# Kernel optimization log

Measured on AMD Instinct MI355X. Metric: run time of the kernel, lower is better.

Reference implementation:

```python
import jax, jax.numpy as jnp
import numpy as np


def _erode3d(v):
    # torch: -F.max_pool3d(-v, 3, stride=1, padding=1)  == 3x3x3 min-pool, SAME padding
    return -jax.lax.reduce_window(-v, -jnp.inf, jax.lax.max,
                                  (1, 1, 3, 3, 3), (1, 1, 1, 1, 1), 'SAME')


def _chamfer(pred, gt):
    # pred [B,N,3], gt [B,M,3]; squared-euclidean pairwise via |p|^2 + |g|^2 - 2 p.g
    p2 = jnp.sum(pred * pred, axis=-1)            # [B,N]
    g2 = jnp.sum(gt * gt, axis=-1)                # [B,M]
    cross = jnp.einsum('bnd,bmd->bnm', pred, gt)  # [B,N,M]
    d = p2[:, :, None] + g2[:, None, :] - 2.0 * cross
    return jnp.mean(jnp.min(d, axis=2)) + jnp.mean(jnp.min(d, axis=1))


def _cldice(pred_volume, gt_volume, smooth=1e-5):
    pred_skel = _erode3d(jax.nn.sigmoid(pred_volume))
    gt_skel = _erode3d(gt_volume)
    inter = jnp.sum(pred_skel * gt_skel, axis=(2, 3, 4))
    psum = jnp.sum(pred_skel, axis=(2, 3, 4))
    gsum = jnp.sum(gt_skel, axis=(2, 3, 4))
    dice = (2.0 * inter + smooth) / (psum + gsum + smooth)
    return 1.0 - jnp.mean(dice)


def _depth_loss(pred, gt, mask, alpha=0.1, beta=10.0):
    B = pred.shape[0]
    # SILog
    g = (jnp.log(pred + alpha) - jnp.log(gt + alpha)).reshape(B, -1)
    g_mean = jnp.mean(g, axis=1)
    g_var = jnp.mean(g * g, axis=1) - g_mean * g_mean  # biased var
    silog = 10.0 * jnp.mean(g_var) + beta * jnp.mean(g_mean ** 2)
    # gradient L1
    pgx = jnp.abs(pred[:, :-1, :] - pred[:, 1:, :])
    pgy = jnp.abs(pred[:, :, :-1] - pred[:, :, 1:])
    ggx = jnp.abs(gt[:, :-1, :] - gt[:, 1:, :])
    ggy = jnp.abs(gt[:, :, :-1] - gt[:, :, 1:])
    grad_l1 = jnp.mean(jnp.abs(pgx - ggx)) + jnp.mean(jnp.abs(pgy - ggy))
    # masked L1
    mask_l1 = jnp.sum(jnp.abs(pred - gt) * mask) / (jnp.sum(mask) + 1e-8)
    return silog + grad_l1 + mask_l1


def setup_inputs() -> dict:
    key = jax.random.key(0)
    ks = jax.random.split(key, 6)
    B, N, M = 2, 8192, 8192
    D, H, W = 64, 128, 128
    DH, DW = 512, 512
    return {
        'pred_centers': jax.random.normal(ks[0], (B, N, 3), jnp.float32),
        'pred_volume': jax.random.normal(ks[1], (B, 1, D, H, W), jnp.float32),
        'pred_depth': jax.random.uniform(ks[2], (B, DH, DW), jnp.float32),
        'gt_points': jax.random.normal(ks[3], (B, M, 3), jnp.float32),
        'gt_volume': jax.random.uniform(ks[4], (B, 1, D, H, W), jnp.float32),
        'gt_depth': jax.random.uniform(ks[5], (B, DH, DW), jnp.float32),
        'depth_mask': jnp.ones((B, DH, DW), jnp.float32),
        'iteration': 10000,
    }


def reference(pred_centers, pred_volume, pred_depth, gt_points, gt_volume,
              gt_depth, depth_mask, iteration):
    gamma1_base, gamma2, gamma3 = 2.0, 0.5, 0.01
    gamma1 = gamma1_base * np.log(max(int(iteration), 1) / 20000.0)
    chamfer = _chamfer(pred_centers, gt_points)
    cldice = _cldice(pred_volume, gt_volume)
    dloss = _depth_loss(pred_depth, gt_depth, depth_mask)
    total = gamma1 * chamfer + gamma2 * cldice + gamma3 * dloss
    return total
```

## Files before the change

kernel.cpp:

```cpp
#include <hip/hip_runtime.h>
#include <math.h>

#define B 2
#define N 8192
#define M 8192
#define NPTS (B*N)
#define VD 64
#define VH 128
#define VW 128
#define VVOX (VD*VH*VW)
#define DHH 512
#define DWW 512
#define DPIX (DHH*DWW)

#define OFF_PACK_P 0
#define OFF_PACK_G 65536
#define OFF_WH_P   131072
#define OFF_WH_G   2228224
#define OFF_CHPART 4325376
#define OFF_PCL    5373952
#define OFF_PDE    5375488
#define OFF_PCH    5377024

__device__ __forceinline__ float blockSum(float v, volatile float* sm) {
    #pragma unroll
    for (int o = 32; o > 0; o >>= 1) v += __shfl_down(v, o, 64);
    int lane = threadIdx.x & 63, wid = threadIdx.x >> 6;
    __syncthreads();
    if (lane == 0) sm[wid] = v;
    __syncthreads();
    return sm[0] + sm[1] + sm[2] + sm[3];
}

__device__ __forceinline__ float min3f(float a, float b, float c) {
    return fminf(a, fminf(b, c));
}

__global__ __launch_bounds__(256) void k_pack(const float* __restrict__ pc,
                                              const float* __restrict__ gp,
                                              float* ws) {
    int i = blockIdx.x * 256 + threadIdx.x;
    if (i >= NPTS) return;
    float x = pc[3*i], y = pc[3*i+1], z = pc[3*i+2];
    ((float4*)(ws + OFF_PACK_P))[i] = make_float4(x, y, z, x*x + y*y + z*z);
    x = gp[3*i]; y = gp[3*i+1]; z = gp[3*i+2];
    ((float4*)(ws + OFF_PACK_G))[i] = make_float4(x, y, z, x*x + y*y + z*z);
}

#define QT 8
#define SEGS 32
#define TSEG (M/SEGS)
__global__ __launch_bounds__(256) void k_chamfer(float* ws) {
    __shared__ float4 tt[TSEG];
    const float4* packP = (const float4*)(ws + OFF_PACK_P);
    const float4* packG = (const float4*)(ws + OFF_PACK_G);
    unsigned int bid = blockIdx.x;
    int dir  = bid >> 8;
    int rem  = bid & 255;
    int seg  = rem >> 3;
    int qblk = rem & 7;
    const float4* Q = dir ? packG : packP;
    const float4* T = dir ? packP : packG;

    int qbase = qblk * (256*QT);
    int b = qbase >> 13;

    tt[threadIdx.x] = T[b*M + seg*TSEG + threadIdx.x];

    float nx[QT], ny[QT], nz[QT], q2[QT], dmin[QT];
    #pragma unroll
    for (int k = 0; k < QT; ++k) {
        float4 qv = Q[qbase + k*256 + threadIdx.x];
        nx[k] = -2.f*qv.x; ny[k] = -2.f*qv.y; nz[k] = -2.f*qv.z;
        q2[k] = qv.w; dmin[k] = INFINITY;
    }
    __syncthreads();

    #pragma unroll 4
    for (int j = 0; j < TSEG; ++j) {
        float4 tv = tt[j];
        #pragma unroll
        for (int k = 0; k < QT; ++k) {
            float d = fmaf(tv.x, nx[k], fmaf(tv.y, ny[k], fmaf(tv.z, nz[k], tv.w)));
            dmin[k] = fminf(dmin[k], d);
        }
    }
    float* part = ws + OFF_CHPART + dir*(SEGS*NPTS) + seg*NPTS + qbase;
    #pragma unroll
    for (int k = 0; k < QT; ++k)
        part[k*256 + threadIdx.x] = dmin[k] + q2[k];
}

__global__ __launch_bounds__(256) void k_redmin(float* ws) {
    __shared__ float sm[4];
    int r   = blockIdx.x;
    int dir = r >> 5;
    int blk = r & 31;
    const float* base = ws + OFF_CHPART + dir*(SEGS*NPTS) + blk*512;
    float s = 0.f;
    #pragma unroll
    for (int u = 0; u < 2; ++u) {
        int t = u*256 + threadIdx.x;
        float m = INFINITY;
        #pragma unroll
        for (int sg = 0; sg < SEGS; ++sg) m = fminf(m, base[sg*NPTS + t]);
        s += m;
    }
    float a = blockSum(s, sm);
    if (threadIdx.x == 0) ws[OFF_PCH + r] = a;
}

__global__ __launch_bounds__(256) void k_erodeA(const float* __restrict__ pv,
                                                const float* __restrict__ gv,
                                                float* ws) {
    int r0 = blockIdx.x * 8 + (threadIdx.x >> 5);
    int q  = threadIdx.x & 31;
    int w  = q * 4;
    int b  = r0 >> 13;
    int rb = r0 & 8191;
    int d  = rb >> 7;
    int h  = rb & 127;
    int rowOff = b*VVOX + d*(VH*VW) + h*VW;
    int up = (h > 0)   ? -VW : 0;
    int dn = (h < 127) ?  VW : 0;

    float4 om[2];
    const float* vols[2] = {pv, gv};
    #pragma unroll
    for (int a = 0; a < 2; ++a) {
        const float* row = vols[a] + rowOff;
        float4 acc = make_float4(INFINITY, INFINITY, INFINITY, INFINITY);
        #pragma unroll
        for (int rr = 0; rr < 3; ++rr) {
            const float* rw = row + (rr == 0 ? up : (rr == 2 ? dn : 0));
            float4 c = *(const float4*)(rw + w);
            float l = (q > 0)  ? rw[w-1] : c.x;
            float r = (q < 31) ? rw[w+4] : c.w;
            acc.x = fminf(acc.x, min3f(l,   c.x, c.y));
            acc.y = fminf(acc.y, min3f(c.x, c.y, c.z));
            acc.z = fminf(acc.z, min3f(c.y, c.z, c.w));
            acc.w = fminf(acc.w, min3f(c.z, c.w, r));
        }
        om[a] = acc;
    }
    ((float4*)(ws + OFF_WH_P + rowOff))[q] = om[0];
    ((float4*)(ws + OFF_WH_G + rowOff))[q] = om[1];
}

__global__ __launch_bounds__(256) void k_erodeB(float* ws) {
    __shared__ float sm[4];
    const float4* whP = (const float4*)(ws + OFF_WH_P);
    const float4* whG = (const float4*)(ws + OFF_WH_G);
    int b   = blockIdx.x >> 8;
    int blk = blockIdx.x & 255;
    float li = 0.f, lp = 0.f, lg = 0.f;
    #pragma unroll
    for (int k = 0; k < 4; ++k) {
        int f4 = b*(VVOX/4) + (blk*4 + k)*256 + threadIdx.x;
        int d  = (f4 >> 12) & 63;
        int up = (d > 0)  ? -4096 : 0;
        int dn = (d < 63) ?  4096 : 0;
        float4 p0 = whP[f4+up], p1 = whP[f4], p2 = whP[f4+dn];
        float4 g0 = whG[f4+up], g1 = whG[f4], g2 = whG[f4+dn];
        float4 mp = make_float4(min3f(p0.x,p1.x,p2.x), min3f(p0.y,p1.y,p2.y),
                                min3f(p0.z,p1.z,p2.z), min3f(p0.w,p1.w,p2.w));
        float4 mg = make_float4(min3f(g0.x,g1.x,g2.x), min3f(g0.y,g1.y,g2.y),
                                min3f(g0.z,g1.z,g2.z), min3f(g0.w,g1.w,g2.w));
        float4 ps = make_float4(1.f/(1.f+__expf(-mp.x)), 1.f/(1.f+__expf(-mp.y)),
                                1.f/(1.f+__expf(-mp.z)), 1.f/(1.f+__expf(-mp.w)));
        li += ps.x*mg.x + ps.y*mg.y + ps.z*mg.z + ps.w*mg.w;
        lp += ps.x + ps.y + ps.z + ps.w;
        lg += mg.x + mg.y + mg.z + mg.w;
    }
    float a;
    float* part = ws + OFF_PCL;
    a = blockSum(li, sm); if (threadIdx.x == 0) part[          blockIdx.x] = a;
    a = blockSum(lp, sm); if (threadIdx.x == 0) part[512     + blockIdx.x] = a;
    a = blockSum(lg, sm); if (threadIdx.x == 0) part[1024    + blockIdx.x] = a;
}

__global__ __launch_bounds__(256) void k_depth(const float* __restrict__ pd,
                                               const float* __restrict__ gd,
                                               const float* __restrict__ mk,
                                               float* ws) {
    __shared__ float sm[4];
    int b   = blockIdx.x >> 7;
    int blk = blockIdx.x & 127;
    const float* pb = pd + b * DPIX;
    const float* gb = gd + b * DPIX;
    const float* mb = mk + b * DPIX;
    float sg = 0, sg2 = 0, gx = 0, gy = 0, num = 0, den = 0;
    #pragma unroll
    for (int k = 0; k < 8; ++k) {
        int idx = (blk*8 + k)*256 + threadIdx.x;
        int h = idx >> 9;
        int w = idx & 511;
        float p = pb[idx], g = gb[idx], m = mb[idx];
        float lgv = logf(p + 0.1f) - logf(g + 0.1f);
        sg += lgv; sg2 += lgv * lgv;
        if (h < DHH - 1) {
            float p2 = pb[idx + DWW], g2 = gb[idx + DWW];
            gx += fabsf(fabsf(p - p2) - fabsf(g - g2));
        }
        if (w < DWW - 1) {
            float p2 = pb[idx + 1], g2 = gb[idx + 1];
            gy += fabsf(fabsf(p - p2) - fabsf(g - g2));
        }
        num += fabsf(p - g) * m;
        den += m;
    }
    float a;
    float* part = ws + OFF_PDE;
    a = blockSum(sg,  sm); if (threadIdx.x == 0) part[       blockIdx.x] = a;
    a = blockSum(sg2, sm); if (threadIdx.x == 0) part[256  + blockIdx.x] = a;
    a = blockSum(gx,  sm); if (threadIdx.x == 0) part[512  + blockIdx.x] = a;
    a = blockSum(gy,  sm); if (threadIdx.x == 0) part[768  + blockIdx.x] = a;
    a = blockSum(num, sm); if (threadIdx.x == 0) part[1024 + blockIdx.x] = a;
    a = blockSum(den, sm); if (threadIdx.x == 0) part[1280 + blockIdx.x] = a;
}

__device__ __forceinline__ float sumRange(const float* p, int n, volatile float* sm) {
    float s = 0.f;
    for (int t = threadIdx.x; t < n; t += 256) s += p[t];
    return blockSum(s, sm);
}

__global__ __launch_bounds__(256) void k_final(const float* ws, const int* iter,
                                               float* out) {
    __shared__ float sm[4];
    float sch = sumRange(ws + OFF_PCH, 64, sm);
    float i0  = sumRange(ws + OFF_PCL,        256, sm);
    float i1  = sumRange(ws + OFF_PCL + 256,  256, sm);
    float p0  = sumRange(ws + OFF_PCL + 512,  256, sm);
    float p1  = sumRange(ws + OFF_PCL + 768,  256, sm);
    float g0  = sumRange(ws + OFF_PCL + 1024, 256, sm);
    float g1  = sumRange(ws + OFF_PCL + 1280, 256, sm);
    float sg0 = sumRange(ws + OFF_PDE,        128, sm);
    float sg1 = sumRange(ws + OFF_PDE + 128,  128, sm);
    float s20 = sumRange(ws + OFF_PDE + 256,  128, sm);
    float s21 = sumRange(ws + OFF_PDE + 384,  128, sm);
    float gx  = sumRange(ws + OFF_PDE + 512,  256, sm);
    float gy  = sumRange(ws + OFF_PDE + 768,  256, sm);
    float num = sumRange(ws + OFF_PDE + 1024, 256, sm);
    float den = sumRange(ws + OFF_PDE + 1280, 256, sm);
    if (threadIdx.x != 0) return;

    float chamfer = sch / (float)NPTS;
    float dsum = (2.f*i0 + 1e-5f) / (p0 + g0 + 1e-5f)
               + (2.f*i1 + 1e-5f) / (p1 + g1 + 1e-5f);
    float cldice = 1.f - 0.5f * dsum;
    float silog = 0.f;
    {
        float gm = sg0 / (float)DPIX;
        float gv = s20 / (float)DPIX - gm*gm;
        silog += 10.f*0.5f*gv + 10.f*0.5f*gm*gm;
        gm = sg1 / (float)DPIX;
        gv = s21 / (float)DPIX - gm*gm;
        silog += 10.f*0.5f*gv + 10.f*0.5f*gm*gm;
    }
    float grad_l1 = gx / (float)(B*(DHH-1)*DWW) + gy / (float)(B*DHH*(DWW-1));
    float mask_l1 = num / (den + 1e-8f);
    float dloss = silog + grad_l1 + mask_l1;
    int it = iter[0]; if (it < 1) it = 1;
    float gamma1 = 2.f * logf((float)it / 20000.f);
    out[0] = gamma1 * chamfer + 0.5f * cldice + 0.01f * dloss;
}

extern "C" void kernel_launch(void* const* d_in, const int* in_sizes, int n_in,
                              void* d_out, int out_size, void* d_ws, size_t ws_size,
                              hipStream_t stream) {
    const float* pc  = (const float*)d_in[0];
    const float* pv  = (const float*)d_in[1];
    const float* pd  = (const float*)d_in[2];
    const float* gp  = (const float*)d_in[3];
    const float* gvv = (const float*)d_in[4];
    const float* gd  = (const float*)d_in[5];
    const float* mk  = (const float*)d_in[6];
    const int*   it  = (const int*)d_in[7];
    float* ws  = (float*)d_ws;
    float* out = (float*)d_out;

    k_pack   <<<64,   256, 0, stream>>>(pc, gp, ws);
    k_chamfer<<<512,  256, 0, stream>>>(ws);
    k_redmin <<<64,   256, 0, stream>>>(ws);
    k_erodeA <<<2048, 256, 0, stream>>>(pv, gvv, ws);
    k_erodeB <<<512,  256, 0, stream>>>(ws);
    k_depth  <<<256,  256, 0, stream>>>(pd, gd, mk, ws);
    k_final  <<<1,    256, 0, stream>>>(ws, it, out);
}
```

Baseline: 144.2 us.

## Merge seven kernels into two phases with last-block ticket final reduction

Folds point packing into the chamfer blocks, runs chamfer, horizontal erosion and depth loss as independent block ranges of one launch, and runs min-reduction and vertical erosion in a second launch. The final scalar reduction is done by whichever block arrives last, chosen with an atomic ticket. This removes five kernel launches and lets independent stages overlap on the GPU. In exchange, the chamfer blocks recompute squared norms from strided xyz loads, and correctness now depends on the ticket being reset in phase 1 and on memory fences.

```diff
diff --git a/kernel.cpp b/kernel.cpp
--- a/kernel.cpp
+++ b/kernel.cpp
@@ -13,14 +13,17 @@
 #define DWW 512
 #define DPIX (DHH*DWW)
 
-#define OFF_PACK_P 0
-#define OFF_PACK_G 65536
-#define OFF_WH_P   131072
-#define OFF_WH_G   2228224
-#define OFF_CHPART 4325376
-#define OFF_PCL    5373952
-#define OFF_PDE    5375488
-#define OFF_PCH    5377024
+#define QT 8
+#define SEGS 32
+#define TSEG (M/SEGS)
+
+#define OFF_WH_P   0
+#define OFF_WH_G   2097152
+#define OFF_CHPART 4194304
+#define OFF_PCL    5242880
+#define OFF_PDE    5244416
+#define OFF_PCH    5245952
+#define OFF_TICKET 5246016
 
 __device__ __forceinline__ float blockSum(float v, volatile float* sm) {
     #pragma unroll
@@ -36,198 +39,199 @@
     return fminf(a, fminf(b, c));
 }
 
-__global__ __launch_bounds__(256) void k_pack(const float* __restrict__ pc,
-                                              const float* __restrict__ gp,
-                                              float* ws) {
-    int i = blockIdx.x * 256 + threadIdx.x;
-    if (i >= NPTS) return;
-    float x = pc[3*i], y = pc[3*i+1], z = pc[3*i+2];
-    ((float4*)(ws + OFF_PACK_P))[i] = make_float4(x, y, z, x*x + y*y + z*z);
-    x = gp[3*i]; y = gp[3*i+1]; z = gp[3*i+2];
-    ((float4*)(ws + OFF_PACK_G))[i] = make_float4(x, y, z, x*x + y*y + z*z);
-}
-
-#define QT 8
-#define SEGS 32
-#define TSEG (M/SEGS)
-__global__ __launch_bounds__(256) void k_chamfer(float* ws) {
-    __shared__ float4 tt[TSEG];
-    const float4* packP = (const float4*)(ws + OFF_PACK_P);
-    const float4* packG = (const float4*)(ws + OFF_PACK_G);
-    unsigned int bid = blockIdx.x;
-    int dir  = bid >> 8;
-    int rem  = bid & 255;
-    int seg  = rem >> 3;
-    int qblk = rem & 7;
-    const float4* Q = dir ? packG : packP;
-    const float4* T = dir ? packP : packG;
-
-    int qbase = qblk * (256*QT);
-    int b = qbase >> 13;
-
-    tt[threadIdx.x] = T[b*M + seg*TSEG + threadIdx.x];
-
-    float nx[QT], ny[QT], nz[QT], q2[QT], dmin[QT];
-    #pragma unroll
-    for (int k = 0; k < QT; ++k) {
-        float4 qv = Q[qbase + k*256 + threadIdx.x];
-        nx[k] = -2.f*qv.x; ny[k] = -2.f*qv.y; nz[k] = -2.f*qv.z;
-        q2[k] = qv.w; dmin[k] = INFINITY;
-    }
-    __syncthreads();
-
-    #pragma unroll 4
-    for (int j = 0; j < TSEG; ++j) {
-        float4 tv = tt[j];
-        #pragma unroll
-        for (int k = 0; k < QT; ++k) {
-            float d = fmaf(tv.x, nx[k], fmaf(tv.y, ny[k], fmaf(tv.z, nz[k], tv.w)));
-            dmin[k] = fminf(dmin[k], d);
-        }
-    }
-    float* part = ws + OFF_CHPART + dir*(SEGS*NPTS) + seg*NPTS + qbase;
-    #pragma unroll
-    for (int k = 0; k < QT; ++k)
-        part[k*256 + threadIdx.x] = dmin[k] + q2[k];
-}
-
-__global__ __launch_bounds__(256) void k_redmin(float* ws) {
-    __shared__ float sm[4];
-    int r   = blockIdx.x;
-    int dir = r >> 5;
-    int blk = r & 31;
-    const float* base = ws + OFF_CHPART + dir*(SEGS*NPTS) + blk*512;
-    float s = 0.f;
-    #pragma unroll
-    for (int u = 0; u < 2; ++u) {
-        int t = u*256 + threadIdx.x;
-        float m = INFINITY;
-        #pragma unroll
-        for (int sg = 0; sg < SEGS; ++sg) m = fminf(m, base[sg*NPTS + t]);
-        s += m;
-    }
-    float a = blockSum(s, sm);
-    if (threadIdx.x == 0) ws[OFF_PCH + r] = a;
-}
-
-__global__ __launch_bounds__(256) void k_erodeA(const float* __restrict__ pv,
-                                                const float* __restrict__ gv,
-                                                float* ws) {
-    int r0 = blockIdx.x * 8 + (threadIdx.x >> 5);
-    int q  = threadIdx.x & 31;
-    int w  = q * 4;
-    int b  = r0 >> 13;
-    int rb = r0 & 8191;
-    int d  = rb >> 7;
-    int h  = rb & 127;
-    int rowOff = b*VVOX + d*(VH*VW) + h*VW;
-    int up = (h > 0)   ? -VW : 0;
-    int dn = (h < 127) ?  VW : 0;
-
-    float4 om[2];
-    const float* vols[2] = {pv, gv};
-    #pragma unroll
-    for (int a = 0; a < 2; ++a) {
-        const float* row = vols[a] + rowOff;
-        float4 acc = make_float4(INFINITY, INFINITY, INFINITY, INFINITY);
-        #pragma unroll
-        for (int rr = 0; rr < 3; ++rr) {
-            const float* rw = row + (rr == 0 ? up : (rr == 2 ? dn : 0));
-            float4 c = *(const float4*)(rw + w);
-            float l = (q > 0)  ? rw[w-1] : c.x;
-            float r = (q < 31) ? rw[w+4] : c.w;
-            acc.x = fminf(acc.x, min3f(l,   c.x, c.y));
-            acc.y = fminf(acc.y, min3f(c.x, c.y, c.z));
-            acc.z = fminf(acc.z, min3f(c.y, c.z, c.w));
-            acc.w = fminf(acc.w, min3f(c.z, c.w, r));
-        }
-        om[a] = acc;
-    }
-    ((float4*)(ws + OFF_WH_P + rowOff))[q] = om[0];
-    ((float4*)(ws + OFF_WH_G + rowOff))[q] = om[1];
-}
-
-__global__ __launch_bounds__(256) void k_erodeB(float* ws) {
-    __shared__ float sm[4];
-    const float4* whP = (const float4*)(ws + OFF_WH_P);
-    const float4* whG = (const float4*)(ws + OFF_WH_G);
-    int b   = blockIdx.x >> 8;
-    int blk = blockIdx.x & 255;
-    float li = 0.f, lp = 0.f, lg = 0.f;
-    #pragma unroll
-    for (int k = 0; k < 4; ++k) {
-        int f4 = b*(VVOX/4) + (blk*4 + k)*256 + threadIdx.x;
-        int d  = (f4 >> 12) & 63;
-        int up = (d > 0)  ? -4096 : 0;
-        int dn = (d < 63) ?  4096 : 0;
-        float4 p0 = whP[f4+up], p1 = whP[f4], p2 = whP[f4+dn];
-        float4 g0 = whG[f4+up], g1 = whG[f4], g2 = whG[f4+dn];
-        float4 mp = make_float4(min3f(p0.x,p1.x,p2.x), min3f(p0.y,p1.y,p2.y),
-                                min3f(p0.z,p1.z,p2.z), min3f(p0.w,p1.w,p2.w));
-        float4 mg = make_float4(min3f(g0.x,g1.x,g2.x), min3f(g0.y,g1.y,g2.y),
-                                min3f(g0.z,g1.z,g2.z), min3f(g0.w,g1.w,g2.w));
-        float4 ps = make_float4(1.f/(1.f+__expf(-mp.x)), 1.f/(1.f+__expf(-mp.y)),
-                                1.f/(1.f+__expf(-mp.z)), 1.f/(1.f+__expf(-mp.w)));
-        li += ps.x*mg.x + ps.y*mg.y + ps.z*mg.z + ps.w*mg.w;
-        lp += ps.x + ps.y + ps.z + ps.w;
-        lg += mg.x + mg.y + mg.z + mg.w;
-    }
-    float a;
-    float* part = ws + OFF_PCL;
-    a = blockSum(li, sm); if (threadIdx.x == 0) part[          blockIdx.x] = a;
-    a = blockSum(lp, sm); if (threadIdx.x == 0) part[512     + blockIdx.x] = a;
-    a = blockSum(lg, sm); if (threadIdx.x == 0) part[1024    + blockIdx.x] = a;
-}
-
-__global__ __launch_bounds__(256) void k_depth(const float* __restrict__ pd,
-                                               const float* __restrict__ gd,
-                                               const float* __restrict__ mk,
-                                               float* ws) {
-    __shared__ float sm[4];
-    int b   = blockIdx.x >> 7;
-    int blk = blockIdx.x & 127;
-    const float* pb = pd + b * DPIX;
-    const float* gb = gd + b * DPIX;
-    const float* mb = mk + b * DPIX;
-    float sg = 0, sg2 = 0, gx = 0, gy = 0, num = 0, den = 0;
-    #pragma unroll
-    for (int k = 0; k < 8; ++k) {
-        int idx = (blk*8 + k)*256 + threadIdx.x;
-        int h = idx >> 9;
-        int w = idx & 511;
-        float p = pb[idx], g = gb[idx], m = mb[idx];
-        float lgv = logf(p + 0.1f) - logf(g + 0.1f);
-        sg += lgv; sg2 += lgv * lgv;
-        if (h < DHH - 1) {
-            float p2 = pb[idx + DWW], g2 = gb[idx + DWW];
-            gx += fabsf(fabsf(p - p2) - fabsf(g - g2));
-        }
-        if (w < DWW - 1) {
-            float p2 = pb[idx + 1], g2 = gb[idx + 1];
-            gy += fabsf(fabsf(p - p2) - fabsf(g - g2));
-        }
-        num += fabsf(p - g) * m;
-        den += m;
-    }
-    float a;
-    float* part = ws + OFF_PDE;
-    a = blockSum(sg,  sm); if (threadIdx.x == 0) part[       blockIdx.x] = a;
-    a = blockSum(sg2, sm); if (threadIdx.x == 0) part[256  + blockIdx.x] = a;
-    a = blockSum(gx,  sm); if (threadIdx.x == 0) part[512  + blockIdx.x] = a;
-    a = blockSum(gy,  sm); if (threadIdx.x == 0) part[768  + blockIdx.x] = a;
-    a = blockSum(num, sm); if (threadIdx.x == 0) part[1024 + blockIdx.x] = a;
-    a = blockSum(den, sm); if (threadIdx.x == 0) part[1280 + blockIdx.x] = a;
-}
-
 __device__ __forceinline__ float sumRange(const float* p, int n, volatile float* sm) {
     float s = 0.f;
     for (int t = threadIdx.x; t < n; t += 256) s += p[t];
     return blockSum(s, sm);
 }
 
-__global__ __launch_bounds__(256) void k_final(const float* ws, const int* iter,
-                                               float* out) {
+__global__ __launch_bounds__(256) void k_phase1(const float* __restrict__ pc,
+                                                const float* __restrict__ gp,
+                                                const float* __restrict__ pv,
+                                                const float* __restrict__ gv,
+                                                const float* __restrict__ pd,
+                                                const float* __restrict__ gd,
+                                                const float* __restrict__ mk,
+                                                float* ws) {
+    __shared__ float4 smem[TSEG];
+    unsigned int bb = blockIdx.x;
+    if (bb == 0 && threadIdx.x == 0) *(int*)(ws + OFF_TICKET) = 0;
+
+    if (bb < 512) {
+        int dir  = bb >> 8;
+        int rem  = bb & 255;
+        int seg  = rem >> 3;
+        int qblk = rem & 7;
+        const float* Q = dir ? gp : pc;
+        const float* T = dir ? pc : gp;
+        int qbase = qblk * (256*QT);
+        int b = qbase >> 13;
+
+        {
+            int t = b*M + seg*TSEG + threadIdx.x;
+            float x = T[3*t], y = T[3*t+1], z = T[3*t+2];
+            smem[threadIdx.x] = make_float4(x, y, z, x*x + y*y + z*z);
+        }
+        float nx[QT], ny[QT], nz[QT], q2[QT], dmin[QT];
+        #pragma unroll
+        for (int k = 0; k < QT; ++k) {
+            int i = qbase + k*256 + threadIdx.x;
+            float x = Q[3*i], y = Q[3*i+1], z = Q[3*i+2];
+            nx[k] = -2.f*x; ny[k] = -2.f*y; nz[k] = -2.f*z;
+            q2[k] = x*x + y*y + z*z; dmin[k] = INFINITY;
+        }
+        __syncthreads();
+        #pragma unroll 4
+        for (int j = 0; j < TSEG; ++j) {
+            float4 tv = smem[j];
+            #pragma unroll
+            for (int k = 0; k < QT; ++k) {
+                float d = fmaf(tv.x, nx[k], fmaf(tv.y, ny[k], fmaf(tv.z, nz[k], tv.w)));
+                dmin[k] = fminf(dmin[k], d);
+            }
+        }
+        float* part = ws + OFF_CHPART + dir*(SEGS*NPTS) + seg*NPTS + qbase;
+        #pragma unroll
+        for (int k = 0; k < QT; ++k)
+            part[k*256 + threadIdx.x] = dmin[k] + q2[k];
+
+    } else if (bb < 2560) {
+        int r0 = (bb - 512) * 8 + (threadIdx.x >> 5);
+        int q  = threadIdx.x & 31;
+        int w  = q * 4;
+        int b  = r0 >> 13;
+        int rb = r0 & 8191;
+        int d  = rb >> 7;
+        int h  = rb & 127;
+        int rowOff = b*VVOX + d*(VH*VW) + h*VW;
+        int up = (h > 0)   ? -VW : 0;
+        int dn = (h < 127) ?  VW : 0;
+
+        float4 om[2];
+        const float* vols[2] = {pv, gv};
+        #pragma unroll
+        for (int a = 0; a < 2; ++a) {
+            const float* row = vols[a] + rowOff;
+            float4 acc = make_float4(INFINITY, INFINITY, INFINITY, INFINITY);
+            #pragma unroll
+            for (int rr = 0; rr < 3; ++rr) {
+                const float* rw = row + (rr == 0 ? up : (rr == 2 ? dn : 0));
+                float4 c = *(const float4*)(rw + w);
+                float l = (q > 0)  ? rw[w-1] : c.x;
+                float r = (q < 31) ? rw[w+4] : c.w;
+                acc.x = fminf(acc.x, min3f(l,   c.x, c.y));
+                acc.y = fminf(acc.y, min3f(c.x, c.y, c.z));
+                acc.z = fminf(acc.z, min3f(c.y, c.z, c.w));
+                acc.w = fminf(acc.w, min3f(c.z, c.w, r));
+            }
+            om[a] = acc;
+        }
+        ((float4*)(ws + OFF_WH_P + rowOff))[q] = om[0];
+        ((float4*)(ws + OFF_WH_G + rowOff))[q] = om[1];
+
+    } else {
+        volatile float* sm = (volatile float*)smem;
+        int idx0 = bb - 2560;
+        int b   = idx0 >> 7;
+        int blk = idx0 & 127;
+        const float* pb = pd + b * DPIX;
+        const float* gb = gd + b * DPIX;
+        const float* mb = mk + b * DPIX;
+        float sg = 0, sg2 = 0, gx = 0, gy = 0, num = 0, den = 0;
+        #pragma unroll
+        for (int k = 0; k < 8; ++k) {
+            int idx = (blk*8 + k)*256 + threadIdx.x;
+            int h = idx >> 9;
+            int w = idx & 511;
+            float p = pb[idx], g = gb[idx], m = mb[idx];
+            float lgv = logf(p + 0.1f) - logf(g + 0.1f);
+            sg += lgv; sg2 += lgv * lgv;
+            if (h < DHH - 1) {
+                float p2 = pb[idx + DWW], g2 = gb[idx + DWW];
+                gx += fabsf(fabsf(p - p2) - fabsf(g - g2));
+            }
+            if (w < DWW - 1) {
+                float p2 = pb[idx + 1], g2 = gb[idx + 1];
+                gy += fabsf(fabsf(p - p2) - fabsf(g - g2));
+            }
+            num += fabsf(p - g) * m;
+            den += m;
+        }
+        float a;
+        float* part = ws + OFF_PDE;
+        a = blockSum(sg,  sm); if (threadIdx.x == 0) part[       idx0] = a;
+        a = blockSum(sg2, sm); if (threadIdx.x == 0) part[256  + idx0] = a;
+        a = blockSum(gx,  sm); if (threadIdx.x == 0) part[512  + idx0] = a;
+        a = blockSum(gy,  sm); if (threadIdx.x == 0) part[768  + idx0] = a;
+        a = blockSum(num, sm); if (threadIdx.x == 0) part[1024 + idx0] = a;
+        a = blockSum(den, sm); if (threadIdx.x == 0) part[1280 + idx0] = a;
+    }
+}
+
+#define P2_BLOCKS 576
+__global__ __launch_bounds__(256) void k_phase2(float* ws, const int* iter,
+                                                float* out) {
     __shared__ float sm[4];
+    __shared__ int amLast;
+    unsigned int bb = blockIdx.x;
+
+    if (bb < 64) {
+        int dir = bb >> 5;
+        int blk = bb & 31;
+        const float* base = ws + OFF_CHPART + dir*(SEGS*NPTS) + blk*512;
+        float s = 0.f;
+        #pragma unroll
+        for (int u = 0; u < 2; ++u) {
+            int t = u*256 + threadIdx.x;
+            float m = INFINITY;
+            #pragma unroll
+            for (int sg = 0; sg < SEGS; ++sg) m = fminf(m, base[sg*NPTS + t]);
+            s += m;
+        }
+        float a = blockSum(s, sm);
+        if (threadIdx.x == 0) ws[OFF_PCH + bb] = a;
+    } else {
+        int idx0 = bb - 64;
+        const float4* whP = (const float4*)(ws + OFF_WH_P);
+        const float4* whG = (const float4*)(ws + OFF_WH_G);
+        int b   = idx0 >> 8;
+        int blk = idx0 & 255;
+        float li = 0.f, lp = 0.f, lg = 0.f;
+        #pragma unroll
+        for (int k = 0; k < 4; ++k) {
+            int f4 = b*(VVOX/4) + (blk*4 + k)*256 + threadIdx.x;
+            int d  = (f4 >> 12) & 63;
+            int up = (d > 0)  ? -4096 : 0;
+            int dn = (d < 63) ?  4096 : 0;
+            float4 p0 = whP[f4+up], p1 = whP[f4], p2 = whP[f4+dn];
+            float4 g0 = whG[f4+up], g1 = whG[f4], g2 = whG[f4+dn];
+            float4 mp = make_float4(min3f(p0.x,p1.x,p2.x), min3f(p0.y,p1.y,p2.y),
+                                    min3f(p0.z,p1.z,p2.z), min3f(p0.w,p1.w,p2.w));
+            float4 mg = make_float4(min3f(g0.x,g1.x,g2.x), min3f(g0.y,g1.y,g2.y),
+                                    min3f(g0.z,g1.z,g2.z), min3f(g0.w,g1.w,g2.w));
+            float4 ps = make_float4(1.f/(1.f+__expf(-mp.x)), 1.f/(1.f+__expf(-mp.y)),
+                                    1.f/(1.f+__expf(-mp.z)), 1.f/(1.f+__expf(-mp.w)));
+            li += ps.x*mg.x + ps.y*mg.y + ps.z*mg.z + ps.w*mg.w;
+            lp += ps.x + ps.y + ps.z + ps.w;
+            lg += mg.x + mg.y + mg.z + mg.w;
+        }
+        float a;
+        float* part = ws + OFF_PCL;
+        a = blockSum(li, sm); if (threadIdx.x == 0) part[        idx0] = a;
+        a = blockSum(lp, sm); if (threadIdx.x == 0) part[512  + idx0] = a;
+        a = blockSum(lg, sm); if (threadIdx.x == 0) part[1024 + idx0] = a;
+    }
+
+    __threadfence();
+    if (threadIdx.x == 0) {
+        int t = __hip_atomic_fetch_add((int*)(ws + OFF_TICKET), 1,
+                                       __ATOMIC_ACQ_REL, __HIP_MEMORY_SCOPE_AGENT);
+        amLast = (t == P2_BLOCKS - 1);
+    }
+    __syncthreads();
+    if (!amLast) return;
+    __threadfence();
+
     float sch = sumRange(ws + OFF_PCH, 64, sm);
     float i0  = sumRange(ws + OFF_PCL,        256, sm);
     float i1  = sumRange(ws + OFF_PCL + 256,  256, sm);
@@ -280,11 +284,6 @@
     float* ws  = (float*)d_ws;
     float* out = (float*)d_out;
 
-    k_pack   <<<64,   256, 0, stream>>>(pc, gp, ws);
-    k_chamfer<<<512,  256, 0, stream>>>(ws);
-    k_redmin <<<64,   256, 0, stream>>>(ws);
-    k_erodeA <<<2048, 256, 0, stream>>>(pv, gvv, ws);
-    k_erodeB <<<512,  256, 0, stream>>>(ws);
-    k_depth  <<<256,  256, 0, stream>>>(pd, gd, mk, ws);
-    k_final  <<<1,    256, 0, stream>>>(ws, it, out);
-}
+    k_phase1<<<2816, 256, 0, stream>>>(pc, gp, pv, gvv, pd, gd, mk, ws);
+    k_phase2<<<P2_BLOCKS, 256, 0, stream>>>(ws, it, out);
+}
```

New measurement: 179.7 us. 24.6% more time.
